# Optimization experiments

Hardware: AMD Instinct MI355X
Metric: run time of the kernel (lower is better)

## Reference

```python
import jax, jax.numpy as jnp
import numpy as np

N_NODES = 100000
N_EDGES = 1600000
IN_DIM = 64
OUT_DIM = 64


def setup_inputs() -> dict:
    key = jax.random.key(0)
    k_x, k_e, k_wm, k_bm, k_wu, k_bu = jax.random.split(key, 6)
    x = jax.random.normal(k_x, (N_NODES, IN_DIM), dtype=jnp.float32)
    edge_index = jax.random.randint(k_e, (2, N_EDGES), 0, N_NODES, dtype=jnp.int64)
    # PyTorch Linear default init: U(-1/sqrt(fan_in), 1/sqrt(fan_in))
    lim_m = 1.0 / np.sqrt(2 * IN_DIM)
    lim_u = 1.0 / np.sqrt(IN_DIM + OUT_DIM)
    W_msg = jax.random.uniform(k_wm, (2 * IN_DIM, OUT_DIM), jnp.float32, -lim_m, lim_m)
    b_msg = jax.random.uniform(k_bm, (OUT_DIM,), jnp.float32, -lim_m, lim_m)
    W_upd = jax.random.uniform(k_wu, (IN_DIM + OUT_DIM, OUT_DIM), jnp.float32, -lim_u, lim_u)
    b_upd = jax.random.uniform(k_bu, (OUT_DIM,), jnp.float32, -lim_u, lim_u)
    return {"x": x, "edge_index": edge_index, "W_msg": W_msg, "b_msg": b_msg,
            "W_upd": W_upd, "b_upd": b_upd}


def reference(x, edge_index, W_msg, b_msg, W_upd, b_upd):
    num_nodes = x.shape[0]
    source, target = edge_index[0], edge_index[1]
    # gather endpoint features and compute messages: [E, 2*in] -> [E, out]
    edge_feats = jnp.concatenate([x[source], x[target]], axis=-1)
    messages = jax.nn.relu(edge_feats @ W_msg + b_msg)
    # mean aggregation onto target nodes
    agg_sum = jax.ops.segment_sum(messages, target, num_segments=num_nodes)
    counts = jax.ops.segment_sum(jnp.ones_like(target, dtype=x.dtype), target,
                                 num_segments=num_nodes)
    aggregated = agg_sum / jnp.clip(counts, 1.0, None)[:, None]
    # update MLP: [N, in+out] -> [N, out]
    updated = jax.nn.relu(jnp.concatenate([x, aggregated], axis=-1) @ W_upd + b_upd)
    return updated
```

## Files before the change

### kernel.cpp

```cpp
#include <hip/hip_runtime.h>
#include <hip/hip_bf16.h>

#define N_NODES 100000
#define N_EDGES 1600000
#define DIM 64
#define NB 196
#define CAP 9216
#define SMASK 0x1FFFFu

typedef __attribute__((ext_vector_type(8))) short bf16x8;
typedef __attribute__((ext_vector_type(4))) float f32x4;
typedef __attribute__((ext_vector_type(2))) float f32x2;

__device__ __forceinline__ float b2f(unsigned int u16) {
    return __uint_as_float(u16 << 16);
}
__device__ __forceinline__ unsigned short f2bs(float f) {
    __hip_bfloat16 h = __float2bfloat16(f);
    return *reinterpret_cast<unsigned short*>(&h);
}

__global__ __launch_bounds__(256) void node_transform(
    const float* __restrict__ x, const float* __restrict__ W_msg,
    const float* __restrict__ b_msg,
    unsigned int* __restrict__ Xs8, uint2* __restrict__ XtP,
    unsigned short* __restrict__ xB, int* __restrict__ bcursor)
{
    __shared__ unsigned short WB[8192];
    const int tid = threadIdx.x;
    const int gtid = blockIdx.x * 256 + tid;
    if (gtid < NB) bcursor[gtid] = gtid * CAP;

    for (int i = tid; i < 8192; i += 256) {
        const int j = i & 7, l = (i >> 3) & 63, kk = (i >> 9) & 1, ct = i >> 10;
        const int k = kk * 32 + ((l >> 4) << 3) + j;
        const int c = ct * 16 + (l & 15);
        WB[i] = f2bs(W_msg[(((c >> 6) << 6) + k) * 64 + (c & 63)]);
    }
    __syncthreads();

    const int lane = tid & 63, w = tid >> 6;
    const int r0 = blockIdx.x * 64 + w * 16;
    if (r0 >= N_NODES) return;

    f32x4 acc[8];
    #pragma unroll
    for (int ct = 0; ct < 8; ++ct) acc[ct] = (f32x4){0.f, 0.f, 0.f, 0.f};

    const int r = r0 + (lane & 15);
    #pragma unroll
    for (int kk = 0; kk < 2; ++kk) {
        const int off = kk * 32 + ((lane >> 4) << 3);
        const float4* xp = reinterpret_cast<const float4*>(&x[r * 64 + off]);
        const float4 p0 = xp[0], p1 = xp[1];
        bf16x8 a;
        a[0] = (short)f2bs(p0.x); a[1] = (short)f2bs(p0.y);
        a[2] = (short)f2bs(p0.z); a[3] = (short)f2bs(p0.w);
        a[4] = (short)f2bs(p1.x); a[5] = (short)f2bs(p1.y);
        a[6] = (short)f2bs(p1.z); a[7] = (short)f2bs(p1.w);
        *reinterpret_cast<bf16x8*>(&xB[r * 64 + off]) = a;
        #pragma unroll
        for (int ct = 0; ct < 8; ++ct) {
            const bf16x8 b = *reinterpret_cast<const bf16x8*>(
                &WB[(((ct << 1) | kk) * 64 + lane) << 3]);
            acc[ct] = __builtin_amdgcn_mfma_f32_16x16x32_bf16(a, b, acc[ct], 0, 0, 0);
        }
    }

    const int fr = lane & 15;
    const int rb = r0 + ((lane >> 4) << 2);
    const float bj0 = b_msg[fr],      bj1 = b_msg[16 + fr];
    const float bj2 = b_msg[32 + fr], bj3 = b_msg[48 + fr];
    #pragma unroll
    for (int q = 0; q < 4; ++q) {
        unsigned int wpk = 0;
        wpk = (unsigned)__builtin_amdgcn_cvt_pk_fp8_f32(acc[0][q], acc[1][q], (int)wpk, false);
        wpk = (unsigned)__builtin_amdgcn_cvt_pk_fp8_f32(acc[2][q], acc[3][q], (int)wpk, true);
        Xs8[(rb + q) * 16 + fr] = wpk;
        uint2 v;
        v.x = (unsigned)f2bs(acc[4][q] + bj0) | ((unsigned)f2bs(acc[5][q] + bj1) << 16);
        v.y = (unsigned)f2bs(acc[6][q] + bj2) | ((unsigned)f2bs(acc[7][q] + bj3) << 16);
        XtP[(rb + q) * 16 + fr] = v;
    }
}

__global__ __launch_bounds__(256) void partition(const int* __restrict__ eidx,
                                                 int* __restrict__ bcursor,
                                                 unsigned int* __restrict__ pairs)
{
    __shared__ unsigned int sbuf[4096];
    __shared__ int dbase[4096];
    __shared__ int tcnt[NB], toff[NB], gpos[NB];
    __shared__ int wsum[4];
    const int tid = threadIdx.x, lane = tid & 63, wid = tid >> 6;
    const int base = blockIdx.x * 4096;
    const int tcount = min(4096, N_EDGES - base);
    if (tid < NB) tcnt[tid] = 0;
    __syncthreads();

    unsigned int pk[16]; int bb[16]; int rk[16];
    #pragma unroll
    for (int j = 0; j < 16; ++j) {
        const int idx = base + j * 256 + tid;
        bb[j] = -1;
        if (idx < N_EDGES) {
            const int sv = eidx[idx];
            const int tv = eidx[N_EDGES + idx];
            bb[j] = tv >> 9;
            pk[j] = (unsigned)sv | ((unsigned)(tv & 511) << 17);
            rk[j] = atomicAdd(&tcnt[bb[j]], 1);
        }
    }
    __syncthreads();

    const int v = (tid < NB) ? tcnt[tid] : 0;
    int s = v;
    #pragma unroll
    for (int d = 1; d < 64; d <<= 1) { int u = __shfl_up(s, d); if (lane >= d) s += u; }
    if (lane == 63) wsum[wid] = s;
    __syncthreads();
    if (wid == 0) {
        int ws = (lane < 4) ? wsum[lane] : 0;
        #pragma unroll
        for (int d = 1; d < 4; d <<= 1) { int u = __shfl_up(ws, d); if (lane >= d) ws += u; }
        if (lane < 4) wsum[lane] = ws;
    }
    __syncthreads();
    const int exc = (wid ? wsum[wid - 1] : 0) + s - v;
    if (tid < NB) {
        toff[tid] = exc;
        gpos[tid] = v ? atomicAdd(&bcursor[tid], v) : 0;
    }
    __syncthreads();

    #pragma unroll
    for (int j = 0; j < 16; ++j) {
        if (bb[j] >= 0) {
            const int l = toff[bb[j]] + rk[j];
            sbuf[l]  = pk[j];
            dbase[l] = gpos[bb[j]] + rk[j];
        }
    }
    __syncthreads();
    for (int i = tid; i < tcount; i += 256)
        pairs[dbase[i]] = sbuf[i];
}

__global__ __launch_bounds__(512) void bucket_sort(const int* __restrict__ bcursor,
                                                   const unsigned int* __restrict__ pairs,
                                                   int* __restrict__ csr,
                                                   int* __restrict__ deg,
                                                   int* __restrict__ row)
{
    __shared__ unsigned int ebuf[CAP];
    __shared__ unsigned short rbuf[CAP];
    __shared__ int ncnt[512], noff[512];
    __shared__ int wsum[8];
    const int tid = threadIdx.x, lane = tid & 63, wid = tid >> 6;
    const int b = blockIdx.x;
    const int s0 = b * CAP;
    const int cnt = bcursor[b] - s0;
    ncnt[tid] = 0;
    __syncthreads();

    for (int i = tid; i < cnt; i += 512) {
        const unsigned int p = pairs[s0 + i];
        ebuf[i] = p;
        rbuf[i] = (unsigned short)atomicAdd(&ncnt[p >> 17], 1);
    }
    __syncthreads();

    const int v = ncnt[tid];
    int s = v;
    #pragma unroll
    for (int d = 1; d < 64; d <<= 1) { int u = __shfl_up(s, d); if (lane >= d) s += u; }
    if (lane == 63) wsum[wid] = s;
    __syncthreads();
    if (wid == 0) {
        int ws = (lane < 8) ? wsum[lane] : 0;
        #pragma unroll
        for (int d = 1; d < 8; d <<= 1) { int u = __shfl_up(ws, d); if (lane >= d) ws += u; }
        if (lane < 8) wsum[lane] = ws;
    }
    __syncthreads();
    const int exc = (wid ? wsum[wid - 1] : 0) + s - v;
    noff[tid] = exc;
    const int n = b * 512 + tid;
    if (n < N_NODES) { deg[n] = v; row[n] = s0 + exc; }
    __syncthreads();

    for (int i = tid; i < cnt; i += 512) {
        const unsigned int p = ebuf[i];
        csr[s0 + noff[p >> 17] + (int)rbuf[i]] = (int)(p & SMASK);
    }
}

__device__ __forceinline__ void acc_fp8(unsigned int u,
    float t0, float t1, float t2, float t3,
    float& a0, float& a1, float& a2, float& a3)
{
    const f32x2 lo = __builtin_amdgcn_cvt_pk_f32_fp8(u, false);
    const f32x2 hi = __builtin_amdgcn_cvt_pk_f32_fp8(u, true);
    a0 += fmaxf(lo.x + t0, 0.f);
    a1 += fmaxf(lo.y + t1, 0.f);
    a2 += fmaxf(hi.x + t2, 0.f);
    a3 += fmaxf(hi.y + t3, 0.f);
}

__global__ __launch_bounds__(256) void aggregate(
    const int* __restrict__ row, const int* __restrict__ deg,
    const int* __restrict__ csr,
    const unsigned int* __restrict__ Xs8, const uint2* __restrict__ XtP,
    uint2* __restrict__ aggP)
{
    const int n = blockIdx.x * 4 + (threadIdx.x >> 6);
    const int lane = threadIdx.x & 63;
    if (n >= N_NODES) return;
    const int c = lane & 15, q = lane >> 4;
    const int start = row[n], d = deg[n];
    const uint2 tp = XtP[n * 16 + c];
    const float t0 = b2f(tp.x & 0xffffu), t1 = b2f(tp.x >> 16);
    const float t2 = b2f(tp.y & 0xffffu), t3 = b2f(tp.y >> 16);
    float a0 = 0.f, a1 = 0.f, a2 = 0.f, a3 = 0.f;
    int i = 0;
    for (; i + 16 <= d; i += 16) {
        const int s0 = csr[start + i + q];
        const int s1 = csr[start + i + 4 + q];
        const int s2 = csr[start + i + 8 + q];
        const int s3 = csr[start + i + 12 + q];
        const unsigned int u0 = Xs8[s0 * 16 + c];
        const unsigned int u1 = Xs8[s1 * 16 + c];
        const unsigned int u2 = Xs8[s2 * 16 + c];
        const unsigned int u3 = Xs8[s3 * 16 + c];
        acc_fp8(u0, t0, t1, t2, t3, a0, a1, a2, a3);
        acc_fp8(u1, t0, t1, t2, t3, a0, a1, a2, a3);
        acc_fp8(u2, t0, t1, t2, t3, a0, a1, a2, a3);
        acc_fp8(u3, t0, t1, t2, t3, a0, a1, a2, a3);
    }
    for (; i + 4 <= d; i += 4) {
        const unsigned int u = Xs8[csr[start + i + q] * 16 + c];
        acc_fp8(u, t0, t1, t2, t3, a0, a1, a2, a3);
    }
    const int rem = d - i;
    if (q < rem) {
        const unsigned int u = Xs8[csr[start + i + q] * 16 + c];
        acc_fp8(u, t0, t1, t2, t3, a0, a1, a2, a3);
    }
    a0 += __shfl_xor(a0, 16); a0 += __shfl_xor(a0, 32);
    a1 += __shfl_xor(a1, 16); a1 += __shfl_xor(a1, 32);
    a2 += __shfl_xor(a2, 16); a2 += __shfl_xor(a2, 32);
    a3 += __shfl_xor(a3, 16); a3 += __shfl_xor(a3, 32);
    if (q == 0) {
        const float inv = (d > 0) ? 1.0f / (float)d : 0.f;
        uint2 v;
        v.x = (unsigned)f2bs(a0 * inv) | ((unsigned)f2bs(a1 * inv) << 16);
        v.y = (unsigned)f2bs(a2 * inv) | ((unsigned)f2bs(a3 * inv) << 16);
        aggP[n * 16 + c] = v;
    }
}

__global__ __launch_bounds__(256) void node_update(
    const unsigned short* __restrict__ xB, const uint2* __restrict__ aggP,
    const float* __restrict__ W_upd, const float* __restrict__ b_upd,
    float* __restrict__ out)
{
    __shared__ unsigned short WB[8192];
    const int tid = threadIdx.x;
    for (int i = tid; i < 8192; i += 256) {
        const int j = i & 7, l = (i >> 3) & 63, kk = (i >> 9) & 3, ct = i >> 11;
        const int hi = l >> 4;
        int k;
        if (kk < 2) k = kk * 32 + (hi << 3) + j;
        else        k = 64 + ((j & 3) << 4) + ((kk - 2) << 3) + (hi << 1) + (j >> 2);
        const int c = ct * 16 + (l & 15);
        WB[i] = f2bs(W_upd[k * 64 + c]);
    }
    __syncthreads();

    const int lane = tid & 63, w = tid >> 6;
    const int r0 = blockIdx.x * 64 + w * 16;
    if (r0 >= N_NODES) return;

    f32x4 acc[4];
    #pragma unroll
    for (int ct = 0; ct < 4; ++ct) acc[ct] = (f32x4){0.f, 0.f, 0.f, 0.f};

    const int r = r0 + (lane & 15);
    const int hi = lane >> 4;
    #pragma unroll
    for (int kk = 0; kk < 4; ++kk) {
        bf16x8 a;
        if (kk < 2) {
            a = *reinterpret_cast<const bf16x8*>(&xB[r * 64 + kk * 32 + (hi << 3)]);
        } else {
            a = *reinterpret_cast<const bf16x8*>(
                &aggP[r * 16 + ((kk - 2) << 3) + (hi << 1)]);
        }
        #pragma unroll
        for (int ct = 0; ct < 4; ++ct) {
            const bf16x8 b = *reinterpret_cast<const bf16x8*>(
                &WB[(((ct << 2) | kk) * 64 + lane) << 3]);
            acc[ct] = __builtin_amdgcn_mfma_f32_16x16x32_bf16(a, b, acc[ct], 0, 0, 0);
        }
    }

    const int rb = r0 + (hi << 2);
    #pragma unroll
    for (int ct = 0; ct < 4; ++ct) {
        const int c = ct * 16 + (lane & 15);
        const float bj = b_upd[c];
        #pragma unroll
        for (int q = 0; q < 4; ++q)
            out[(rb + q) * 64 + c] = fmaxf(acc[ct][q] + bj, 0.f);
    }
}

extern "C" void kernel_launch(void* const* d_in, const int* in_sizes, int n_in,
                              void* d_out, int out_size, void* d_ws, size_t ws_size,
                              hipStream_t stream) {
    const float* x     = (const float*)d_in[0];
    const int*   eidx  = (const int*)  d_in[1];
    const float* W_msg = (const float*)d_in[2];
    const float* b_msg = (const float*)d_in[3];
    const float* W_upd = (const float*)d_in[4];
    const float* b_upd = (const float*)d_in[5];
    float* out = (float*)d_out;

    int* deg     = (int*)d_ws;
    int* row     = deg + N_NODES;
    int* bcursor = row + N_NODES;
    unsigned int* pairs = (unsigned int*)(bcursor + 256);
    int* csr     = (int*)(pairs + NB * CAP);
    unsigned int* Xs8 = (unsigned int*)(csr + NB * CAP);
    uint2* XtP   = (uint2*)(Xs8 + (size_t)N_NODES * 16);
    unsigned short* xB = (unsigned short*)(XtP + (size_t)N_NODES * 16);
    uint2* aggP  = (uint2*)(xB + (size_t)N_NODES * DIM);

    const int nodeBlocks = (N_NODES + 63) / 64;
    const int partBlocks = (N_EDGES + 4095) / 4096;

    node_transform<<<nodeBlocks, 256, 0, stream>>>(x, W_msg, b_msg, Xs8, XtP, xB, bcursor);
    partition<<<partBlocks, 256, 0, stream>>>(eidx, bcursor, pairs);
    bucket_sort<<<NB, 512, 0, stream>>>(bcursor, pairs, csr, deg, row);
    aggregate<<<(N_NODES + 3) / 4, 256, 0, stream>>>(row, deg, csr,
        Xs8, XtP, aggP);
    node_update<<<nodeBlocks, 256, 0, stream>>>(xB, aggP, W_upd, b_upd, out);
}
```

Before: 122.4 us.

## Fuse aggregation into node update via LDS and store target term as fp8

Merges the aggregate and node_update kernels into one: each wave aggregates 16 nodes sequentially, writes the bf16 means to shared memory, then runs the update MFMA reading them from LDS. This removes the global aggP round trip and one launch. The target-side message term (including bias) is also stored in fp8 instead of bf16, halving that buffer. In exchange there are fewer waves in flight during the latency-bound gather (1563 blocks each handling 64 nodes instead of 4 per block), serial per-wave node loops with load imbalance, and lower precision on the target term.

New measurement: 148.4 us. 1.21x slower.

```diff
diff --git a/kernel.cpp b/kernel.cpp
--- a/kernel.cpp
+++ b/kernel.cpp
@@ -12,9 +12,6 @@
 typedef __attribute__((ext_vector_type(4))) float f32x4;
 typedef __attribute__((ext_vector_type(2))) float f32x2;
 
-__device__ __forceinline__ float b2f(unsigned int u16) {
-    return __uint_as_float(u16 << 16);
-}
 __device__ __forceinline__ unsigned short f2bs(float f) {
     __hip_bfloat16 h = __float2bfloat16(f);
     return *reinterpret_cast<unsigned short*>(&h);
@@ -23,7 +20,7 @@
 __global__ __launch_bounds__(256) void node_transform(
     const float* __restrict__ x, const float* __restrict__ W_msg,
     const float* __restrict__ b_msg,
-    unsigned int* __restrict__ Xs8, uint2* __restrict__ XtP,
+    unsigned int* __restrict__ Xs8, unsigned int* __restrict__ Xt8,
     unsigned short* __restrict__ xB, int* __restrict__ bcursor)
 {
     __shared__ unsigned short WB[8192];
@@ -73,14 +70,14 @@
     const float bj2 = b_msg[32 + fr], bj3 = b_msg[48 + fr];
     #pragma unroll
     for (int q = 0; q < 4; ++q) {
-        unsigned int wpk = 0;
-        wpk = (unsigned)__builtin_amdgcn_cvt_pk_fp8_f32(acc[0][q], acc[1][q], (int)wpk, false);
-        wpk = (unsigned)__builtin_amdgcn_cvt_pk_fp8_f32(acc[2][q], acc[3][q], (int)wpk, true);
-        Xs8[(rb + q) * 16 + fr] = wpk;
-        uint2 v;
-        v.x = (unsigned)f2bs(acc[4][q] + bj0) | ((unsigned)f2bs(acc[5][q] + bj1) << 16);
-        v.y = (unsigned)f2bs(acc[6][q] + bj2) | ((unsigned)f2bs(acc[7][q] + bj3) << 16);
-        XtP[(rb + q) * 16 + fr] = v;
+        unsigned int xs = 0;
+        xs = (unsigned)__builtin_amdgcn_cvt_pk_fp8_f32(acc[0][q], acc[1][q], (int)xs, false);
+        xs = (unsigned)__builtin_amdgcn_cvt_pk_fp8_f32(acc[2][q], acc[3][q], (int)xs, true);
+        Xs8[(rb + q) * 16 + fr] = xs;
+        unsigned int xt = 0;
+        xt = (unsigned)__builtin_amdgcn_cvt_pk_fp8_f32(acc[4][q] + bj0, acc[5][q] + bj1, (int)xt, false);
+        xt = (unsigned)__builtin_amdgcn_cvt_pk_fp8_f32(acc[6][q] + bj2, acc[7][q] + bj3, (int)xt, true);
+        Xt8[(rb + q) * 16 + fr] = xt;
     }
 }
 
@@ -207,64 +204,17 @@
     a3 += fmaxf(hi.y + t3, 0.f);
 }
 
-__global__ __launch_bounds__(256) void aggregate(
+__global__ __launch_bounds__(256) void agg_update(
     const int* __restrict__ row, const int* __restrict__ deg,
     const int* __restrict__ csr,
-    const unsigned int* __restrict__ Xs8, const uint2* __restrict__ XtP,
-    uint2* __restrict__ aggP)
-{
-    const int n = blockIdx.x * 4 + (threadIdx.x >> 6);
-    const int lane = threadIdx.x & 63;
-    if (n >= N_NODES) return;
-    const int c = lane & 15, q = lane >> 4;
-    const int start = row[n], d = deg[n];
-    const uint2 tp = XtP[n * 16 + c];
-    const float t0 = b2f(tp.x & 0xffffu), t1 = b2f(tp.x >> 16);
-    const float t2 = b2f(tp.y & 0xffffu), t3 = b2f(tp.y >> 16);
-    float a0 = 0.f, a1 = 0.f, a2 = 0.f, a3 = 0.f;
-    int i = 0;
-    for (; i + 16 <= d; i += 16) {
-        const int s0 = csr[start + i + q];
-        const int s1 = csr[start + i + 4 + q];
-        const int s2 = csr[start + i + 8 + q];
-        const int s3 = csr[start + i + 12 + q];
-        const unsigned int u0 = Xs8[s0 * 16 + c];
-        const unsigned int u1 = Xs8[s1 * 16 + c];
-        const unsigned int u2 = Xs8[s2 * 16 + c];
-        const unsigned int u3 = Xs8[s3 * 16 + c];
-        acc_fp8(u0, t0, t1, t2, t3, a0, a1, a2, a3);
-        acc_fp8(u1, t0, t1, t2, t3, a0, a1, a2, a3);
-        acc_fp8(u2, t0, t1, t2, t3, a0, a1, a2, a3);
-        acc_fp8(u3, t0, t1, t2, t3, a0, a1, a2, a3);
-    }
-    for (; i + 4 <= d; i += 4) {
-        const unsigned int u = Xs8[csr[start + i + q] * 16 + c];
-        acc_fp8(u, t0, t1, t2, t3, a0, a1, a2, a3);
-    }
-    const int rem = d - i;
-    if (q < rem) {
-        const unsigned int u = Xs8[csr[start + i + q] * 16 + c];
-        acc_fp8(u, t0, t1, t2, t3, a0, a1, a2, a3);
-    }
-    a0 += __shfl_xor(a0, 16); a0 += __shfl_xor(a0, 32);
-    a1 += __shfl_xor(a1, 16); a1 += __shfl_xor(a1, 32);
-    a2 += __shfl_xor(a2, 16); a2 += __shfl_xor(a2, 32);
-    a3 += __shfl_xor(a3, 16); a3 += __shfl_xor(a3, 32);
-    if (q == 0) {
-        const float inv = (d > 0) ? 1.0f / (float)d : 0.f;
-        uint2 v;
-        v.x = (unsigned)f2bs(a0 * inv) | ((unsigned)f2bs(a1 * inv) << 16);
-        v.y = (unsigned)f2bs(a2 * inv) | ((unsigned)f2bs(a3 * inv) << 16);
-        aggP[n * 16 + c] = v;
-    }
-}
-
-__global__ __launch_bounds__(256) void node_update(
-    const unsigned short* __restrict__ xB, const uint2* __restrict__ aggP,
+    const unsigned int* __restrict__ Xs8, const unsigned int* __restrict__ Xt8,
+    const unsigned short* __restrict__ xB,
     const float* __restrict__ W_upd, const float* __restrict__ b_upd,
     float* __restrict__ out)
 {
     __shared__ unsigned short WB[8192];
+    __shared__ uint2 aggLDS[64][18];
+
     const int tid = threadIdx.x;
     for (int i = tid; i < 8192; i += 256) {
         const int j = i & 7, l = (i >> 3) & 63, kk = (i >> 9) & 3, ct = i >> 11;
@@ -275,18 +225,67 @@
         const int c = ct * 16 + (l & 15);
         WB[i] = f2bs(W_upd[k * 64 + c]);
     }
-    __syncthreads();
 
     const int lane = tid & 63, w = tid >> 6;
-    const int r0 = blockIdx.x * 64 + w * 16;
-    if (r0 >= N_NODES) return;
+    const int n0 = blockIdx.x * 64;
+    const int r0w = n0 + w * 16;
+    const int c = lane & 15, q = lane >> 4;
+
+    if (r0w < N_NODES) {
+        for (int j = 0; j < 16; ++j) {
+            const int n = r0w + j;
+            const int start = row[n], d = deg[n];
+            const unsigned int tp = Xt8[n * 16 + c];
+            const f32x2 tlo = __builtin_amdgcn_cvt_pk_f32_fp8(tp, false);
+            const f32x2 thi = __builtin_amdgcn_cvt_pk_f32_fp8(tp, true);
+            const float t0 = tlo.x, t1 = tlo.y, t2 = thi.x, t3 = thi.y;
+            float a0 = 0.f, a1 = 0.f, a2 = 0.f, a3 = 0.f;
+            int i = 0;
+            for (; i + 16 <= d; i += 16) {
+                const int s0 = csr[start + i + q];
+                const int s1 = csr[start + i + 4 + q];
+                const int s2 = csr[start + i + 8 + q];
+                const int s3 = csr[start + i + 12 + q];
+                const unsigned int u0 = Xs8[s0 * 16 + c];
+                const unsigned int u1 = Xs8[s1 * 16 + c];
+                const unsigned int u2 = Xs8[s2 * 16 + c];
+                const unsigned int u3 = Xs8[s3 * 16 + c];
+                acc_fp8(u0, t0, t1, t2, t3, a0, a1, a2, a3);
+                acc_fp8(u1, t0, t1, t2, t3, a0, a1, a2, a3);
+                acc_fp8(u2, t0, t1, t2, t3, a0, a1, a2, a3);
+                acc_fp8(u3, t0, t1, t2, t3, a0, a1, a2, a3);
+            }
+            for (; i + 4 <= d; i += 4) {
+                const unsigned int u = Xs8[csr[start + i + q] * 16 + c];
+                acc_fp8(u, t0, t1, t2, t3, a0, a1, a2, a3);
+            }
+            const int rem = d - i;
+            if (q < rem) {
+                const unsigned int u = Xs8[csr[start + i + q] * 16 + c];
+                acc_fp8(u, t0, t1, t2, t3, a0, a1, a2, a3);
+            }
+            a0 += __shfl_xor(a0, 16); a0 += __shfl_xor(a0, 32);
+            a1 += __shfl_xor(a1, 16); a1 += __shfl_xor(a1, 32);
+            a2 += __shfl_xor(a2, 16); a2 += __shfl_xor(a2, 32);
+            a3 += __shfl_xor(a3, 16); a3 += __shfl_xor(a3, 32);
+            if (q == 0) {
+                const float inv = (d > 0) ? 1.0f / (float)d : 0.f;
+                uint2 v;
+                v.x = (unsigned)f2bs(a0 * inv) | ((unsigned)f2bs(a1 * inv) << 16);
+                v.y = (unsigned)f2bs(a2 * inv) | ((unsigned)f2bs(a3 * inv) << 16);
+                aggLDS[w * 16 + j][c] = v;
+            }
+        }
+    }
+    __syncthreads();
+    if (r0w >= N_NODES) return;
 
     f32x4 acc[4];
     #pragma unroll
     for (int ct = 0; ct < 4; ++ct) acc[ct] = (f32x4){0.f, 0.f, 0.f, 0.f};
 
-    const int r = r0 + (lane & 15);
-    const int hi = lane >> 4;
+    const int fr = lane & 15, hi = lane >> 4;
+    const int r = r0w + fr;
     #pragma unroll
     for (int kk = 0; kk < 4; ++kk) {
         bf16x8 a;
@@ -294,7 +293,7 @@
             a = *reinterpret_cast<const bf16x8*>(&xB[r * 64 + kk * 32 + (hi << 3)]);
         } else {
             a = *reinterpret_cast<const bf16x8*>(
-                &aggP[r * 16 + ((kk - 2) << 3) + (hi << 1)]);
+                &aggLDS[w * 16 + fr][((kk - 2) << 3) + (hi << 1)]);
         }
         #pragma unroll
         for (int ct = 0; ct < 4; ++ct) {
@@ -304,14 +303,14 @@
         }
     }
 
-    const int rb = r0 + (hi << 2);
+    const int rb = r0w + (hi << 2);
     #pragma unroll
     for (int ct = 0; ct < 4; ++ct) {
-        const int c = ct * 16 + (lane & 15);
-        const float bj = b_upd[c];
-        #pragma unroll
-        for (int q = 0; q < 4; ++q)
-            out[(rb + q) * 64 + c] = fmaxf(acc[ct][q] + bj, 0.f);
+        const int cc = ct * 16 + fr;
+        const float bj = b_upd[cc];
+        #pragma unroll
+        for (int qq = 0; qq < 4; ++qq)
+            out[(rb + qq) * 64 + cc] = fmaxf(acc[ct][qq] + bj, 0.f);
     }
 }
 
@@ -332,17 +331,15 @@
     unsigned int* pairs = (unsigned int*)(bcursor + 256);
     int* csr     = (int*)(pairs + NB * CAP);
     unsigned int* Xs8 = (unsigned int*)(csr + NB * CAP);
-    uint2* XtP   = (uint2*)(Xs8 + (size_t)N_NODES * 16);
-    unsigned short* xB = (unsigned short*)(XtP + (size_t)N_NODES * 16);
-    uint2* aggP  = (uint2*)(xB + (size_t)N_NODES * DIM);
+    unsigned int* Xt8 = Xs8 + (size_t)N_NODES * 16;
+    unsigned short* xB = (unsigned short*)(Xt8 + (size_t)N_NODES * 16);
 
     const int nodeBlocks = (N_NODES + 63) / 64;
     const int partBlocks = (N_EDGES + 4095) / 4096;
 
-    node_transform<<<nodeBlocks, 256, 0, stream>>>(x, W_msg, b_msg, Xs8, XtP, xB, bcursor);
+    node_transform<<<nodeBlocks, 256, 0, stream>>>(x, W_msg, b_msg, Xs8, Xt8, xB, bcursor);
     partition<<<partBlocks, 256, 0, stream>>>(eidx, bcursor, pairs);
     bucket_sort<<<NB, 512, 0, stream>>>(bcursor, pairs, csr, deg, row);
-    aggregate<<<(N_NODES + 3) / 4, 256, 0, stream>>>(row, deg, csr,
-        Xs8, XtP, aggP);
-    node_update<<<nodeBlocks, 256, 0, stream>>>(xB, aggP, W_upd, b_upd, out);
-}
+    agg_update<<<nodeBlocks, 256, 0, stream>>>(row, deg, csr, Xs8, Xt8, xB,
+                                               W_upd, b_upd, out);
+}
```
